# Kernel optimization log

Hardware: AMD Instinct MI355X
Metric: run time of the kernel (lower is better)

Reference implementation:

```python
import jax, jax.numpy as jnp
import numpy as np

DT = 0.005
BETA = 0.9
THR = 0.5
TAU_MIN = 0.02
TAU_STEP = 0.03
TAU_R = 0.002
SLOPE = 25.0  # snntorch fast_sigmoid default surrogate slope

@jax.custom_vjp
def spike_fn(x):
    return (x > 0).astype(x.dtype)

def _spike_fwd(x):
    return spike_fn(x), x

def _spike_bwd(x, g):
    return (g / (SLOPE * jnp.abs(x) + 1.0) ** 2,)

spike_fn.defvjp(_spike_fwd, _spike_bwd)

def setup_inputs() -> dict:
    key = jax.random.key(0)
    ks = jax.random.split(key, 8)
    T, NIN, H, NOUT, P = 1000, 4, 4096, 2, 16
    inv_sqrt_h = 1.0 / np.sqrt(H).astype(np.float32)
    return {
        "x": jax.random.normal(ks[0], (T, NIN + 2, 1), jnp.float32),
        "noise": jax.random.normal(ks[1], (T, H, 1), jnp.float32),
        "Win": jax.random.normal(ks[2], (H, NIN + 2), jnp.float32),
        "Wout": jax.random.normal(ks[3], (NOUT, H), jnp.float32) * inv_sqrt_h,
        "pin": jax.random.normal(ks[4], (H, P), jnp.float32) * inv_sqrt_h,
        "pout": jax.random.normal(ks[5], (H, P), jnp.float32) * inv_sqrt_h,
        "l": jax.random.normal(ks[6], (P,), jnp.float32) * inv_sqrt_h,
        "sigmoid_tau_d": jax.random.normal(ks[7], (H, 1), jnp.float32),
    }

def reference(x, noise, Win, Wout, pin, pout, l, sigmoid_tau_d):
    H = Win.shape[0]
    tau_d = jax.nn.sigmoid(sigmoid_tau_d) * TAU_STEP + TAU_MIN   # [H,1]
    Wr = (l * pin) @ pout.T                                      # [H,H] low-rank recurrent matrix
    decay_r = jnp.exp(jnp.asarray(-DT / TAU_R, x.dtype))         # scalar
    decay_d = jnp.exp(-DT / tau_d)                               # [H,1]
    s_gain = DT / (tau_d * TAU_R)                                # [H,1]

    def step(carry, inp):
        mem, r, s = carry
        xi, ni = inp
        I = Win @ xi + Wr @ r + ni / 10.0                        # [H,1]
        # snntorch Leaky, reset_mechanism='subtract': reset from incoming mem (detached)
        reset = jax.lax.stop_gradient(spike_fn(mem - THR))
        mem = BETA * mem + I - reset * THR
        spk = spike_fn(mem - THR)
        s = s * decay_r + s_gain * spk
        r = decay_d * r + DT * s
        return (mem, r, s), r

    z = jnp.zeros((H, 1), x.dtype)
    _, R = jax.lax.scan(step, (z, z, z), (x, noise))             # R: [T,H,1]
    y = jnp.einsum('oh,thj->toj', Wout, R)                       # [T,O,1]
    return y
```

## Files before the change

kernel.cpp:

```cpp
#include <hip/hip_runtime.h>
#include <math.h>

#define KB       4
#define NBOOT    32
#define NTHREADS 256
#define NW       4
#define HID      4096
#define HB       (HID / KB)
#define NPT      4
#define TT       1000
#define PP       16
#define SLOTW    32

#define BETA 0.9f
#define THRV 0.5f
#define DTV  0.005f

template<int CTRL>
__device__ __forceinline__ float dppx(float v) {
    return __int_as_float(__builtin_amdgcn_update_dpp(
        0, __float_as_int(v), CTRL, 0xF, 0xF, true));
}

__device__ __forceinline__ unsigned long long AL(const unsigned long long* p) {
    return __hip_atomic_load(p, __ATOMIC_RELAXED, __HIP_MEMORY_SCOPE_AGENT);
}
__device__ __forceinline__ void AS(unsigned long long* p, unsigned long long v) {
    __hip_atomic_store(p, v, __ATOMIC_RELAXED, __HIP_MEMORY_SCOPE_AGENT);
}
__device__ __forceinline__ void st64_sc0(unsigned long long* p, unsigned long long v) {
    asm volatile("global_store_dwordx2 %0, %1, off sc0" :: "v"(p), "v"(v) : "memory");
}
__device__ __forceinline__ void ld64x3_sc0(const unsigned long long* p0,
                                           const unsigned long long* p1,
                                           const unsigned long long* p2,
                                           unsigned long long& v0,
                                           unsigned long long& v1,
                                           unsigned long long& v2) {
    asm volatile("global_load_dwordx2 %0, %3, off sc0\n\t"
                 "global_load_dwordx2 %1, %4, off sc0\n\t"
                 "global_load_dwordx2 %2, %5, off sc0\n\t"
                 "s_waitcnt vmcnt(0)"
                 : "=&v"(v0), "=&v"(v1), "=&v"(v2)
                 : "v"(p0), "v"(p1), "v"(p2) : "memory");
}

__global__ void zero_kernel(unsigned* boot) {
    int i = threadIdx.x;
    if (i < NBOOT) boot[i] = 0u;
}

__global__ __launch_bounds__(NTHREADS, 1)
void snn_kernel(const float* __restrict__ x,
                const float* __restrict__ noise,
                const float* __restrict__ Win,
                const float* __restrict__ Wout,
                const float* __restrict__ pin,
                const float* __restrict__ pout,
                const float* __restrict__ lvec,
                const float* __restrict__ stdv,
                float* __restrict__ out,
                unsigned long long* __restrict__ slotsL2,
                unsigned long long* __restrict__ slotsAG,
                unsigned* __restrict__ boot)
{
    const int tid  = threadIdx.x;
    const int wave = tid >> 6;
    const int lane = tid & 63;

    unsigned xcc;
    asm volatile("s_getreg_b32 %0, hwreg(HW_REG_XCC_ID)" : "=s"(xcc));
    if (tid == 0)
        __hip_atomic_store(&boot[blockIdx.x], 0x80000000u | (xcc & 0xffu),
                           __ATOMIC_RELAXED, __HIP_MEMORY_SCOPE_AGENT);
    unsigned e = 0;
    if (lane < NBOOT) {
        int sp = 0;
        do {
            e = __hip_atomic_load(&boot[lane], __ATOMIC_RELAXED,
                                  __HIP_MEMORY_SCOPE_AGENT);
        } while (!(e & 0x80000000u) && ++sp < (1 << 22));
    }
    unsigned long long m = 0; int found = -1;
    #pragma unroll 1
    for (int c = 0; c < 8; ++c) {
        unsigned long long bm = __ballot(lane < NBOOT && (e & 0xffu) == (unsigned)c);
        if (found < 0 && __popcll(bm) >= KB) { m = bm; found = c; }
    }
    const int below = __popcll(m & ((1ull << blockIdx.x) - 1ull));
    const bool chosen = (found >= 0) && ((m >> blockIdx.x) & 1ull) && (below < KB);
    if (!chosen) return;
    const int b = below;

    const int h0 = b * HB + tid * NPT;

    const bool lb0 = (lane & 1) != 0;
    const bool lb1 = (lane & 2) != 0;
    const bool lb2 = (lane & 4) != 0;
    const bool lb3 = (lane & 8) != 0;

    const int rbA = (b == 0) ? 1 : 0;
    const int rbB = (b <= 1) ? 2 : 1;
    const int rbC = (b <= 2) ? 3 : 2;

    __shared__ float part[NW][20];
    __shared__ float ubuf[NW][16];

    float lv[PP];
    #pragma unroll
    for (int p = 0; p < PP; p += 4) {
        float4 t4 = *(const float4*)&lvec[p];
        lv[p] = t4.x; lv[p+1] = t4.y; lv[p+2] = t4.z; lv[p+3] = t4.w;
    }
    float pl[NPT][PP], po[NPT][PP];
    #pragma unroll
    for (int j = 0; j < NPT; ++j) {
        #pragma unroll
        for (int p = 0; p < PP; p += 4) {
            float4 a = *(const float4*)&pin[(h0+j)*PP + p];
            pl[j][p]   = a.x*lv[p];   pl[j][p+1] = a.y*lv[p+1];
            pl[j][p+2] = a.z*lv[p+2]; pl[j][p+3] = a.w*lv[p+3];
            float4 e4 = *(const float4*)&pout[(h0+j)*PP + p];
            po[j][p]   = e4.x; po[j][p+1] = e4.y;
            po[j][p+2] = e4.z; po[j][p+3] = e4.w;
        }
    }
    float win[NPT][6];
    #pragma unroll
    for (int j = 0; j < NPT; ++j) {
        const float2* wr = (const float2*)&Win[(h0+j)*6];
        float2 wA = wr[0], wB = wr[1], wC = wr[2];
        win[j][0]=wA.x; win[j][1]=wA.y; win[j][2]=wB.x;
        win[j][3]=wB.y; win[j][4]=wC.x; win[j][5]=wC.y;
    }
    float4 woa = *(const float4*)&Wout[h0];
    float4 wob = *(const float4*)&Wout[HID + h0];

    float4 sd4 = *(const float4*)&stdv[h0];
    float dd[NPT], sg[NPT];
    {
        float sdv[4] = { sd4.x, sd4.y, sd4.z, sd4.w };
        #pragma unroll
        for (int j = 0; j < NPT; ++j) {
            float sig = 1.f / (1.f + expf(-sdv[j]));
            float tau = sig * 0.03f + 0.02f;
            dd[j] = expf(-DTV / tau);
            sg[j] = DTV / (tau * 0.002f);
        }
    }
    const float DECAY_R = expf(-2.5f);

    float mem[NPT], rr[NPT], ss[NPT];
    #pragma unroll
    for (int j = 0; j < NPT; ++j) { mem[j] = 0.f; rr[j] = 0.f; ss[j] = 0.f; }

    const float2* x2 = (const float2*)x;
    float4 nz = *(const float4*)&noise[h0];
    float2 xa = x2[0], xb = x2[1], xc = x2[2];

    float uu[16];
    #pragma unroll
    for (int p = 0; p < 16; ++p) uu[p] = 0.f;

    int use_sc0 = 1;

    for (int t = 0; t <= TT; ++t) {
        float4 nz_n = nz; float2 xa_n = xa, xb_n = xb, xc_n = xc;
        if (t < TT - 1) {
            const int tn = t + 1;
            nz_n = *(const float4*)&noise[tn * HID + h0];
            xa_n = x2[tn*3]; xb_n = x2[tn*3+1]; xc_n = x2[tn*3+2];
        }

        if (t > 0) {
            const int par = t & 1;
            float pa[18];
            #pragma unroll
            for (int p = 0; p < PP; ++p)
                pa[p] = (po[0][p]*rr[0] + po[1][p]*rr[1])
                      + (po[2][p]*rr[2] + po[3][p]*rr[3]);
            pa[16] = (woa.x*rr[0] + woa.y*rr[1]) + (woa.z*rr[2] + woa.w*rr[3]);
            pa[17] = (wob.x*rr[0] + wob.y*rr[1]) + (wob.z*rr[2] + wob.w*rr[3]);

            float a1[8], yv;
            #pragma unroll
            for (int k = 0; k < 8; ++k) {
                float keep = lb0 ? pa[2*k+1] : pa[2*k];
                float send = lb0 ? pa[2*k]   : pa[2*k+1];
                a1[k] = keep + dppx<0xB1>(send);
            }
            {
                float keep = lb0 ? pa[17] : pa[16];
                float send = lb0 ? pa[16] : pa[17];
                yv = keep + dppx<0xB1>(send);
            }
            float a2[4];
            #pragma unroll
            for (int k = 0; k < 4; ++k) {
                float keep = lb1 ? a1[2*k+1] : a1[2*k];
                float send = lb1 ? a1[2*k]   : a1[2*k+1];
                a2[k] = keep + dppx<0x4E>(send);
            }
            yv += dppx<0x4E>(yv);
            float a3[2];
            #pragma unroll
            for (int k = 0; k < 2; ++k) {
                float keep = lb2 ? a2[2*k+1] : a2[2*k];
                float send = lb2 ? a2[2*k]   : a2[2*k+1];
                a3[k] = keep + __shfl_xor(send, 4, 64);
            }
            yv += __shfl_xor(yv, 4, 64);
            float uv;
            {
                float keep = lb3 ? a3[1] : a3[0];
                float send = lb3 ? a3[0] : a3[1];
                uv = keep + dppx<0x128>(send);
            }
            yv += dppx<0x128>(yv);
            uv += __shfl_xor(uv, 16, 64);
            uv += __shfl_xor(uv, 32, 64);
            yv += __shfl_xor(yv, 16, 64);
            yv += __shfl_xor(yv, 32, 64);

            if (lane < 18) part[wave][lane] = (lane < 16) ? uv : yv;
            __syncthreads();

            float bs = 0.f;
            if (lane < 18) {
                bs = (part[0][lane] + part[1][lane])
                   + (part[2][lane] + part[3][lane]);
            }

            if (wave == 0 && lane < 18) {
                union { float f; unsigned u; } cv; cv.f = bs;
                unsigned long long pk = ((unsigned long long)(unsigned)t << 32)
                                      | (unsigned long long)cv.u;
                const size_t si = (size_t)(par*KB + b)*SLOTW + lane;
                st64_sc0(&slotsL2[si], pk);
                AS(&slotsAG[si], pk);
            }

            if (t < TT || b == 0) {
                float f0 = 0.f, f1 = 0.f, f2 = 0.f;
                if (lane < 18) {
                    const size_t sb = (size_t)par * KB;
                    unsigned long long va = 0, vb = 0, vc = 0;
                    bool got = false;
                    if (use_sc0) {
                        const unsigned long long* pa_ = &slotsL2[(sb + rbA)*SLOTW + lane];
                        const unsigned long long* pb_ = &slotsL2[(sb + rbB)*SLOTW + lane];
                        const unsigned long long* pc_ = &slotsL2[(sb + rbC)*SLOTW + lane];
                        int sp = 0;
                        do {
                            ld64x3_sc0(pa_, pb_, pc_, va, vb, vc);
                            got = ((unsigned)(va >> 32) == (unsigned)t)
                                & ((unsigned)(vb >> 32) == (unsigned)t)
                                & ((unsigned)(vc >> 32) == (unsigned)t);
                        } while (!got && ++sp < 256);
                        if (!got) use_sc0 = 0;
                    }
                    if (!got) {
                        const unsigned long long* pa_ = &slotsAG[(sb + rbA)*SLOTW + lane];
                        const unsigned long long* pb_ = &slotsAG[(sb + rbB)*SLOTW + lane];
                        const unsigned long long* pc_ = &slotsAG[(sb + rbC)*SLOTW + lane];
                        int sp2 = 0;
                        do {
                            va = AL(pa_); vb = AL(pb_); vc = AL(pc_);
                        } while ((((unsigned)(va >> 32) != (unsigned)t) |
                                  ((unsigned)(vb >> 32) != (unsigned)t) |
                                  ((unsigned)(vc >> 32) != (unsigned)t)) &&
                                 ++sp2 < (1 << 20));
                    }
                    union { unsigned u; float f; } c0, c1, c2;
                    c0.u = (unsigned)va; c1.u = (unsigned)vb; c2.u = (unsigned)vc;
                    f0 = c0.f; f1 = c1.f; f2 = c2.f;
                }
                float total = (b < 2) ? ((bs + f0) + (f1 + f2))
                                      : ((f0 + f1) + (f2 + bs));
                if (lane < 16) ubuf[wave][lane] = total;
                if (b == 0 && wave == 0 && lane >= 16 && lane < 18)
                    out[(t-1)*2 + (lane - 16)] = total;

                float4 u0 = *(const float4*)&ubuf[wave][0];
                float4 u1 = *(const float4*)&ubuf[wave][4];
                float4 u2 = *(const float4*)&ubuf[wave][8];
                float4 u3 = *(const float4*)&ubuf[wave][12];
                uu[0]=u0.x; uu[1]=u0.y; uu[2]=u0.z; uu[3]=u0.w;
                uu[4]=u1.x; uu[5]=u1.y; uu[6]=u1.z; uu[7]=u1.w;
                uu[8]=u2.x; uu[9]=u2.y; uu[10]=u2.z; uu[11]=u2.w;
                uu[12]=u3.x; uu[13]=u3.y; uu[14]=u3.z; uu[15]=u3.w;
            }
        }

        if (t < TT) {
            float nzv[4] = { nz.x, nz.y, nz.z, nz.w };
            #pragma unroll
            for (int j = 0; j < NPT; ++j) {
                float ra = pl[j][0]*uu[0];
                float rb2_ = pl[j][8]*uu[8];
                #pragma unroll
                for (int p = 1; p < 8; ++p) {
                    ra   += pl[j][p]*uu[p];
                    rb2_ += pl[j][p+8]*uu[p+8];
                }
                float rec = ra + rb2_;
                float xw = win[j][0]*xa.x + win[j][1]*xa.y
                         + win[j][2]*xb.x + win[j][3]*xb.y
                         + win[j][4]*xc.x + win[j][5]*xc.y;
                float I = (xw + rec) + nzv[j] / 10.0f;

                float rst = (mem[j] - THRV > 0.f) ? THRV : 0.f;
                mem[j] = BETA*mem[j] + I - rst;
                float spk = (mem[j] - THRV > 0.f) ? 1.f : 0.f;
                ss[j] = ss[j]*DECAY_R + sg[j]*spk;
                rr[j] = dd[j]*rr[j] + DTV*ss[j];
            }
            nz = nz_n; xa = xa_n; xb = xb_n; xc = xc_n;
        }
    }
}

extern "C" void kernel_launch(void* const* d_in, const int* in_sizes, int n_in,
                              void* d_out, int out_size, void* d_ws, size_t ws_size,
                              hipStream_t stream)
{
    const float* x     = (const float*)d_in[0];
    const float* noise = (const float*)d_in[1];
    const float* Win   = (const float*)d_in[2];
    const float* Wout  = (const float*)d_in[3];
    const float* pin   = (const float*)d_in[4];
    const float* pout  = (const float*)d_in[5];
    const float* l     = (const float*)d_in[6];
    const float* stdv  = (const float*)d_in[7];
    float* out = (float*)d_out;
    unsigned long long* slotsL2 = (unsigned long long*)d_ws;
    unsigned long long* slotsAG = (unsigned long long*)((char*)d_ws + 2048);
    unsigned* boot = (unsigned*)((char*)d_ws + 4096);

    hipLaunchKernelGGL(zero_kernel, dim3(1), dim3(64), 0, stream, boot);
    hipLaunchKernelGGL(snn_kernel, dim3(NBOOT), dim3(NTHREADS), 0, stream,
                       x, noise, Win, Wout, pin, pout, l, stdv,
                       out, slotsL2, slotsAG, boot);
}
```

Measured before the change: 1.644 ms.

## Poll peer partials via atomic RMW and precompute input terms before the wait

Peer partial sums are now polled with global atomic add-zero operations instead of sc0 loads. The intent is that each poll reads the current value in L2 rather than a stale cached copy. The input projection, noise, leak and reset terms are computed before the cross-block wait, so that arithmetic overlaps the synchronisation latency. The poll budget is reduced and the fallback decision is made wave-uniform. Workspace offsets are spread apart and a default block mask is added for when XCC grouping fails. Atomic RMW polling adds extra L2 traffic and could contend with the peer stores.

```diff
diff --git a/kernel.cpp b/kernel.cpp
--- a/kernel.cpp
+++ b/kernel.cpp
@@ -31,18 +31,20 @@
 __device__ __forceinline__ void st64_sc0(unsigned long long* p, unsigned long long v) {
     asm volatile("global_store_dwordx2 %0, %1, off sc0" :: "v"(p), "v"(v) : "memory");
 }
-__device__ __forceinline__ void ld64x3_sc0(const unsigned long long* p0,
-                                           const unsigned long long* p1,
-                                           const unsigned long long* p2,
-                                           unsigned long long& v0,
-                                           unsigned long long& v1,
-                                           unsigned long long& v2) {
-    asm volatile("global_load_dwordx2 %0, %3, off sc0\n\t"
-                 "global_load_dwordx2 %1, %4, off sc0\n\t"
-                 "global_load_dwordx2 %2, %5, off sc0\n\t"
+__device__ __forceinline__ void rmw3_sc0(unsigned long long* p0,
+                                         unsigned long long* p1,
+                                         unsigned long long* p2,
+                                         unsigned long long& v0,
+                                         unsigned long long& v1,
+                                         unsigned long long& v2) {
+    unsigned long long z = 0;
+    asm volatile("global_atomic_add_x2 %0, %3, %6, off sc0\n\t"
+                 "global_atomic_add_x2 %1, %4, %6, off sc0\n\t"
+                 "global_atomic_add_x2 %2, %5, %6, off sc0\n\t"
                  "s_waitcnt vmcnt(0)"
                  : "=&v"(v0), "=&v"(v1), "=&v"(v2)
-                 : "v"(p0), "v"(p1), "v"(p2) : "memory");
+                 : "v"(p0), "v"(p1), "v"(p2), "v"(z)
+                 : "memory");
 }
 
 __global__ void zero_kernel(unsigned* boot) {
@@ -87,8 +89,9 @@
         unsigned long long bm = __ballot(lane < NBOOT && (e & 0xffu) == (unsigned)c);
         if (found < 0 && __popcll(bm) >= KB) { m = bm; found = c; }
     }
+    if (found < 0) m = 0xFull;
     const int below = __popcll(m & ((1ull << blockIdx.x) - 1ull));
-    const bool chosen = (found >= 0) && ((m >> blockIdx.x) & 1ull) && (below < KB);
+    const bool chosen = ((m >> blockIdx.x) & 1ull) && (below < KB);
     if (!chosen) return;
     const int b = below;
 
@@ -150,7 +153,7 @@
     }
     const float DECAY_R = expf(-2.5f);
 
-    float mem[NPT], rr[NPT], ss[NPT];
+    float mem[NPT], rr[NPT], ss[NPT], pre[NPT];
     #pragma unroll
     for (int j = 0; j < NPT; ++j) { mem[j] = 0.f; rr[j] = 0.f; ss[j] = 0.f; }
 
@@ -172,8 +175,9 @@
             xa_n = x2[tn*3]; xb_n = x2[tn*3+1]; xc_n = x2[tn*3+2];
         }
 
+        float bs = 0.f;
+        const int par = t & 1;
         if (t > 0) {
-            const int par = t & 1;
             float pa[18];
             #pragma unroll
             for (int p = 0; p < PP; ++p)
@@ -225,7 +229,6 @@
             if (lane < 18) part[wave][lane] = (lane < 16) ? uv : yv;
             __syncthreads();
 
-            float bs = 0.f;
             if (lane < 18) {
                 bs = (part[0][lane] + part[1][lane])
                    + (part[2][lane] + part[3][lane]);
@@ -239,61 +242,78 @@
                 st64_sc0(&slotsL2[si], pk);
                 AS(&slotsAG[si], pk);
             }
-
-            if (t < TT || b == 0) {
-                float f0 = 0.f, f1 = 0.f, f2 = 0.f;
-                if (lane < 18) {
-                    const size_t sb = (size_t)par * KB;
-                    unsigned long long va = 0, vb = 0, vc = 0;
-                    bool got = false;
-                    if (use_sc0) {
-                        const unsigned long long* pa_ = &slotsL2[(sb + rbA)*SLOTW + lane];
-                        const unsigned long long* pb_ = &slotsL2[(sb + rbB)*SLOTW + lane];
-                        const unsigned long long* pc_ = &slotsL2[(sb + rbC)*SLOTW + lane];
-                        int sp = 0;
-                        do {
-                            ld64x3_sc0(pa_, pb_, pc_, va, vb, vc);
-                            got = ((unsigned)(va >> 32) == (unsigned)t)
-                                & ((unsigned)(vb >> 32) == (unsigned)t)
-                                & ((unsigned)(vc >> 32) == (unsigned)t);
-                        } while (!got && ++sp < 256);
-                        if (!got) use_sc0 = 0;
-                    }
-                    if (!got) {
-                        const unsigned long long* pa_ = &slotsAG[(sb + rbA)*SLOTW + lane];
-                        const unsigned long long* pb_ = &slotsAG[(sb + rbB)*SLOTW + lane];
-                        const unsigned long long* pc_ = &slotsAG[(sb + rbC)*SLOTW + lane];
-                        int sp2 = 0;
-                        do {
-                            va = AL(pa_); vb = AL(pb_); vc = AL(pc_);
-                        } while ((((unsigned)(va >> 32) != (unsigned)t) |
-                                  ((unsigned)(vb >> 32) != (unsigned)t) |
-                                  ((unsigned)(vc >> 32) != (unsigned)t)) &&
-                                 ++sp2 < (1 << 20));
-                    }
-                    union { unsigned u; float f; } c0, c1, c2;
-                    c0.u = (unsigned)va; c1.u = (unsigned)vb; c2.u = (unsigned)vc;
-                    f0 = c0.f; f1 = c1.f; f2 = c2.f;
-                }
-                float total = (b < 2) ? ((bs + f0) + (f1 + f2))
-                                      : ((f0 + f1) + (f2 + bs));
-                if (lane < 16) ubuf[wave][lane] = total;
-                if (b == 0 && wave == 0 && lane >= 16 && lane < 18)
-                    out[(t-1)*2 + (lane - 16)] = total;
-
-                float4 u0 = *(const float4*)&ubuf[wave][0];
-                float4 u1 = *(const float4*)&ubuf[wave][4];
-                float4 u2 = *(const float4*)&ubuf[wave][8];
-                float4 u3 = *(const float4*)&ubuf[wave][12];
-                uu[0]=u0.x; uu[1]=u0.y; uu[2]=u0.z; uu[3]=u0.w;
-                uu[4]=u1.x; uu[5]=u1.y; uu[6]=u1.z; uu[7]=u1.w;
-                uu[8]=u2.x; uu[9]=u2.y; uu[10]=u2.z; uu[11]=u2.w;
-                uu[12]=u3.x; uu[13]=u3.y; uu[14]=u3.z; uu[15]=u3.w;
-            }
         }
 
         if (t < TT) {
             float nzv[4] = { nz.x, nz.y, nz.z, nz.w };
+            #pragma unroll
+            for (int j = 0; j < NPT; ++j) {
+                float xw = win[j][0]*xa.x + win[j][1]*xa.y
+                         + win[j][2]*xb.x + win[j][3]*xb.y
+                         + win[j][4]*xc.x + win[j][5]*xc.y;
+                float rst = (mem[j] - THRV > 0.f) ? THRV : 0.f;
+                pre[j] = BETA*mem[j] + xw + nzv[j] / 10.0f - rst;
+            }
+        }
+
+        if (t > 0 && (t < TT || b == 0)) {
+            const size_t sb = (size_t)par * KB;
+            float f0 = 0.f, f1 = 0.f, f2 = 0.f;
+            unsigned long long va = 0, vb = 0, vc = 0;
+            if (use_sc0) {
+                int got = 1;
+                if (lane < 18) {
+                    unsigned long long* pa_ = &slotsL2[(sb + rbA)*SLOTW + lane];
+                    unsigned long long* pb_ = &slotsL2[(sb + rbB)*SLOTW + lane];
+                    unsigned long long* pc_ = &slotsL2[(sb + rbC)*SLOTW + lane];
+                    const int K = (t == 1) ? 1024 : 64;
+                    int sp = 0, ok;
+                    do {
+                        rmw3_sc0(pa_, pb_, pc_, va, vb, vc);
+                        ok = ((unsigned)(va >> 32) == (unsigned)t)
+                           & ((unsigned)(vb >> 32) == (unsigned)t)
+                           & ((unsigned)(vc >> 32) == (unsigned)t);
+                    } while (!ok && ++sp < K);
+                    got = ok;
+                }
+                if (!__all(got)) use_sc0 = 0;
+            }
+            if (!use_sc0) {
+                if (lane < 18) {
+                    const unsigned long long* pa_ = &slotsAG[(sb + rbA)*SLOTW + lane];
+                    const unsigned long long* pb_ = &slotsAG[(sb + rbB)*SLOTW + lane];
+                    const unsigned long long* pc_ = &slotsAG[(sb + rbC)*SLOTW + lane];
+                    int sp2 = 0;
+                    do {
+                        va = AL(pa_); vb = AL(pb_); vc = AL(pc_);
+                    } while ((((unsigned)(va >> 32) != (unsigned)t) |
+                              ((unsigned)(vb >> 32) != (unsigned)t) |
+                              ((unsigned)(vc >> 32) != (unsigned)t)) &&
+                             ++sp2 < (1 << 20));
+                }
+            }
+            if (lane < 18) {
+                union { unsigned u; float f; } c0, c1, c2;
+                c0.u = (unsigned)va; c1.u = (unsigned)vb; c2.u = (unsigned)vc;
+                f0 = c0.f; f1 = c1.f; f2 = c2.f;
+            }
+            float total = (b < 2) ? ((bs + f0) + (f1 + f2))
+                                  : ((f0 + f1) + (f2 + bs));
+            if (lane < 16) ubuf[wave][lane] = total;
+            if (b == 0 && wave == 0 && lane >= 16 && lane < 18)
+                out[(t-1)*2 + (lane - 16)] = total;
+
+            float4 u0 = *(const float4*)&ubuf[wave][0];
+            float4 u1 = *(const float4*)&ubuf[wave][4];
+            float4 u2 = *(const float4*)&ubuf[wave][8];
+            float4 u3 = *(const float4*)&ubuf[wave][12];
+            uu[0]=u0.x; uu[1]=u0.y; uu[2]=u0.z; uu[3]=u0.w;
+            uu[4]=u1.x; uu[5]=u1.y; uu[6]=u1.z; uu[7]=u1.w;
+            uu[8]=u2.x; uu[9]=u2.y; uu[10]=u2.z; uu[11]=u2.w;
+            uu[12]=u3.x; uu[13]=u3.y; uu[14]=u3.z; uu[15]=u3.w;
+        }
+
+        if (t < TT) {
             #pragma unroll
             for (int j = 0; j < NPT; ++j) {
                 float ra = pl[j][0]*uu[0];
@@ -304,13 +324,7 @@
                     rb2_ += pl[j][p+8]*uu[p+8];
                 }
                 float rec = ra + rb2_;
-                float xw = win[j][0]*xa.x + win[j][1]*xa.y
-                         + win[j][2]*xb.x + win[j][3]*xb.y
-                         + win[j][4]*xc.x + win[j][5]*xc.y;
-                float I = (xw + rec) + nzv[j] / 10.0f;
-
-                float rst = (mem[j] - THRV > 0.f) ? THRV : 0.f;
-                mem[j] = BETA*mem[j] + I - rst;
+                mem[j] = pre[j] + rec;
                 float spk = (mem[j] - THRV > 0.f) ? 1.f : 0.f;
                 ss[j] = ss[j]*DECAY_R + sg[j]*spk;
                 rr[j] = dd[j]*rr[j] + DTV*ss[j];
@@ -334,8 +348,8 @@
     const float* stdv  = (const float*)d_in[7];
     float* out = (float*)d_out;
     unsigned long long* slotsL2 = (unsigned long long*)d_ws;
-    unsigned long long* slotsAG = (unsigned long long*)((char*)d_ws + 2048);
-    unsigned* boot = (unsigned*)((char*)d_ws + 4096);
+    unsigned long long* slotsAG = (unsigned long long*)((char*)d_ws + 4096);
+    unsigned* boot = (unsigned*)((char*)d_ws + 8192);
 
     hipLaunchKernelGGL(zero_kernel, dim3(1), dim3(64), 0, stream, boot);
     hipLaunchKernelGGL(snn_kernel, dim3(NBOOT), dim3(NTHREADS), 0, stream,
```

New measurement: 1.629 ms. About the same (-0.9%).
